# Optimization experiments

Measured on AMD Instinct MI355X. Metric: run time of the kernel, lower is better.

## Reference

```python
import jax, jax.numpy as jnp
import numpy as np

B = 8
N1, N2 = 65536, 16384
C1, C2 = 256, 512
BN_EPS = 1e-5


def setup_inputs() -> dict:
    key = jax.random.key(0)
    ks = jax.random.split(key, 8)
    xyz1 = jax.random.normal(ks[0], (N1, 3), dtype=jnp.float32)
    points1 = jax.random.normal(ks[1], (N1, C1), dtype=jnp.float32)
    xyz2 = jax.random.normal(ks[2], (N2, 3), dtype=jnp.float32)
    points2 = jax.random.normal(ks[3], (N2, C2), dtype=jnp.float32)
    offset1 = (jnp.arange(1, B + 1, dtype=jnp.int32) * (N1 // B))
    offset2 = (jnp.arange(1, B + 1, dtype=jnp.int32) * (N2 // B))
    W1 = jax.random.normal(ks[4], (C1 + C2, 256), dtype=jnp.float32) * 0.02
    b1 = jnp.zeros((256,), jnp.float32)
    g1 = jnp.ones((256,), jnp.float32)
    be1 = jnp.zeros((256,), jnp.float32)
    W2 = jax.random.normal(ks[5], (256, 256), dtype=jnp.float32) * 0.02
    b2 = jnp.zeros((256,), jnp.float32)
    g2 = jnp.ones((256,), jnp.float32)
    be2 = jnp.zeros((256,), jnp.float32)
    return dict(xyz1=xyz1, points1=points1, xyz2=xyz2, points2=points2,
                offset1=offset1, offset2=offset2,
                W1=W1, b1=b1, g1=g1, be1=be1, W2=W2, b2=b2, g2=g2, be2=be2)


def _knn3(q, k):
    # q: [n1,3] queries, k: [n2,3] reference set -> 3-NN idx + euclidean dist
    d2 = (jnp.sum(q * q, -1)[:, None] + jnp.sum(k * k, -1)[None, :]
          - 2.0 * (q @ k.T))                      # [n1, n2]
    neg_d2, idx = jax.lax.top_k(-d2, 3)           # [n1, 3]
    dist = jnp.sqrt(jnp.maximum(-neg_d2, 0.0))
    return idx, dist


def _bn_relu(x, g, be):
    # BatchNorm1d in training mode: biased batch stats over the point dim
    mu = jnp.mean(x, axis=0)
    var = jnp.mean((x - mu) ** 2, axis=0)
    return jax.nn.relu(g * (x - mu) * jax.lax.rsqrt(var + BN_EPS) + be)


def reference(xyz1, points1, xyz2, points2, offset1, offset2,
              W1, b1, g1, be1, W2, b2, g2, be2):
    bsz = offset1.shape[0]
    n1 = xyz1.shape[0] // bsz
    n2 = xyz2.shape[0] // bsz
    q = xyz1.reshape(bsz, n1, 3)
    k = xyz2.reshape(bsz, n2, 3)
    idx, dist = jax.vmap(_knn3)(q, k)             # [B,n1,3], [B,n1,3]
    gidx = (idx + (jnp.arange(bsz, dtype=idx.dtype) * n2)[:, None, None])
    gidx = gidx.reshape(-1, 3)                    # [N1,3] global row ids
    dist = dist.reshape(-1, 3)
    dist_recip = 1.0 / (dist + 1e-8)
    weight = dist_recip / jnp.sum(dist_recip, axis=1, keepdims=True)
    # fused gather + weighted accumulate: [N1,3,C2] * [N1,3,1] -> [N1,C2]
    interpolated = jnp.sum(points2[gidx] * weight[..., None], axis=1)
    x = jnp.concatenate([points1, interpolated], axis=1)  # [N1, C1+C2]
    x = _bn_relu(x @ W1 + b1, g1, be1)
    x = _bn_relu(x @ W2 + b2, g2, be2)
    return x
```

## Files before the change

kernel.cpp:

```cpp
#include <hip/hip_runtime.h>
#include <math.h>

#define N1T 65536
#define N2T 16384
#define BSZ 8
#define N1B 8192
#define N2B 2048
#define C1 256
#define C2 512
#define K1 768
#define HID 256
#define BN_EPS 1e-5f

typedef short bf16x8 __attribute__((ext_vector_type(8)));
typedef float f32x4 __attribute__((ext_vector_type(4)));

__device__ __forceinline__ float mul_rn(float a, float b) {
    float r; asm("v_mul_f32 %0, %1, %2" : "=v"(r) : "v"(a), "v"(b)); return r;
}
__device__ __forceinline__ float add_rn(float a, float b) {
    float r; asm("v_add_f32 %0, %1, %2" : "=v"(r) : "v"(a), "v"(b)); return r;
}
__device__ __forceinline__ float sub_rn(float a, float b) {
    float r; asm("v_sub_f32 %0, %1, %2" : "=v"(r) : "v"(a), "v"(b)); return r;
}
__device__ __forceinline__ float fma_rn(float a, float b, float c) {
    float r; asm("v_fma_f32 %0, %1, %2, %3" : "=v"(r) : "v"(a), "v"(b), "v"(c)); return r;
}
__device__ __forceinline__ short f2bf(float f) {
    unsigned u = __builtin_bit_cast(unsigned, f);
    u += 0x7fffu + ((u >> 16) & 1u);
    return (short)(u >> 16);
}
__device__ __forceinline__ float bf2f(short s) {
    return __builtin_bit_cast(float, ((unsigned)(unsigned short)s) << 16);
}

__global__ __launch_bounds__(256) void knn_kernel(
    const float* __restrict__ xyz1, const float* __restrict__ xyz2,
    int* __restrict__ idx_out, float* __restrict__ w_out)
{
    __shared__ float4 sref[N2B + 4];
    const int tid = threadIdx.x;
    const int qbase = blockIdx.x * 64;
    const int batch = qbase / N1B;
    const float* k2 = xyz2 + (size_t)batch * N2B * 3;
    for (int p = tid; p < N2B; p += 256) {
        float x = k2[3 * p], y = k2[3 * p + 1], z = k2[3 * p + 2];
        float kk = add_rn(add_rn(mul_rn(x, x), mul_rn(y, y)), mul_rn(z, z));
        sref[p + (p >> 9)] = make_float4(x, y, z, kk);
    }
    __syncthreads();

    const int q = qbase + (tid >> 2);
    const int sub = tid & 3;
    const float qx = xyz1[q * 3 + 0], qy = xyz1[q * 3 + 1], qz = xyz1[q * 3 + 2];
    const float qq = add_rn(add_rn(mul_rn(qx, qx), mul_rn(qy, qy)), mul_rn(qz, qz));

    const int base = sub * 513;
    const int gbase = sub * 512;
    float a0 = 1e30f, a1 = 1e30f, a2 = 1e30f;
    int   ai0 = 0x7fffffff, ai1 = 0x7fffffff, ai2 = 0x7fffffff;
    float c0 = 1e30f, c1 = 1e30f, c2 = 1e30f;
    int   ci0 = 0x7fffffff, ci1 = 0x7fffffff, ci2 = 0x7fffffff;
    for (int jj = 0; jj < 256; ++jj) {
        float4 rA = sref[base + jj];
        float4 rB = sref[base + 256 + jj];
        float pA = mul_rn(qx, rA.x);
        float tA = fma_rn(qz, rA.z, fma_rn(qy, rA.y, pA));
        float dA = add_rn(sub_rn(qq, add_rn(tA, tA)), rA.w);
        float pB = mul_rn(qx, rB.x);
        float tB = fma_rn(qz, rB.z, fma_rn(qy, rB.y, pB));
        float dB = add_rn(sub_rn(qq, add_rn(tB, tB)), rB.w);
        if (dA < a2) {
            if (dA < a1) {
                a2 = a1; ai2 = ai1;
                if (dA < a0) { a1 = a0; ai1 = ai0; a0 = dA; ai0 = gbase + jj; }
                else         { a1 = dA; ai1 = gbase + jj; }
            } else { a2 = dA; ai2 = gbase + jj; }
        }
        if (dB < c2) {
            if (dB < c1) {
                c2 = c1; ci2 = ci1;
                if (dB < c0) { c1 = c0; ci1 = ci0; c0 = dB; ci0 = gbase + 256 + jj; }
                else         { c1 = dB; ci1 = gbase + 256 + jj; }
            } else { c2 = dB; ci2 = gbase + 256 + jj; }
        }
    }
    float bd0 = a0, bd1 = a1, bd2 = a2;
    int   bi0 = ai0, bi1 = ai1, bi2 = ai2;
#define LEXINS(d, ji)                                                        \
    if ((d < bd2) || (d == bd2 && ji < bi2)) {                               \
        if ((d < bd1) || (d == bd1 && ji < bi1)) {                           \
            bd2 = bd1; bi2 = bi1;                                            \
            if ((d < bd0) || (d == bd0 && ji < bi0)) {                       \
                bd1 = bd0; bi1 = bi0; bd0 = d; bi0 = ji;                     \
            } else { bd1 = d; bi1 = ji; }                                    \
        } else { bd2 = d; bi2 = ji; }                                        \
    }
    LEXINS(c0, ci0) LEXINS(c1, ci1) LEXINS(c2, ci2)
#pragma unroll
    for (int mask = 1; mask <= 2; mask <<= 1) {
        float pd0 = __shfl_xor(bd0, mask, 64);
        float pd1 = __shfl_xor(bd1, mask, 64);
        float pd2 = __shfl_xor(bd2, mask, 64);
        int   pi0 = __shfl_xor(bi0, mask, 64);
        int   pi1 = __shfl_xor(bi1, mask, 64);
        int   pi2 = __shfl_xor(bi2, mask, 64);
        LEXINS(pd0, pi0) LEXINS(pd1, pi1) LEXINS(pd2, pi2)
    }
#undef LEXINS
    if (sub == 0) {
        float d0s = __fsqrt_rn(fmaxf(bd0, 0.0f));
        float d1s = __fsqrt_rn(fmaxf(bd1, 0.0f));
        float d2s = __fsqrt_rn(fmaxf(bd2, 0.0f));
        float r0 = __fdiv_rn(1.0f, add_rn(d0s, 1e-8f));
        float r1 = __fdiv_rn(1.0f, add_rn(d1s, 1e-8f));
        float r2 = __fdiv_rn(1.0f, add_rn(d2s, 1e-8f));
        float rs = add_rn(add_rn(r0, r1), r2);
        w_out[q * 3 + 0] = __fdiv_rn(r0, rs);
        w_out[q * 3 + 1] = __fdiv_rn(r1, rs);
        w_out[q * 3 + 2] = __fdiv_rn(r2, rs);
        idx_out[q * 3 + 0] = batch * N2B + bi0;
        idx_out[q * 3 + 1] = batch * N2B + bi1;
        idx_out[q * 3 + 2] = batch * N2B + bi2;
    }
}

__global__ __launch_bounds__(256) void cast_p2_kernel(
    const float* __restrict__ p2, short* __restrict__ p2b)
{
    const size_t i = ((size_t)blockIdx.x * 256 + threadIdx.x) * 8;
    float4 u0 = *(const float4*)(p2 + i);
    float4 u1 = *(const float4*)(p2 + i + 4);
    bf16x8 v;
    v[0] = f2bf(u0.x); v[1] = f2bf(u0.y); v[2] = f2bf(u0.z); v[3] = f2bf(u0.w);
    v[4] = f2bf(u1.x); v[5] = f2bf(u1.y); v[6] = f2bf(u1.z); v[7] = f2bf(u1.w);
    *(bf16x8*)(p2b + i) = v;
}

__global__ __launch_bounds__(256) void transpose_w_kernel(
    const float* __restrict__ Win, short* __restrict__ WT, int K, int N)
{
    const int e = blockIdx.x * 256 + threadIdx.x;
    const int k = e / N, n = e % N;
    WT[(size_t)n * K + k] = f2bf(Win[e]);
}

#define LDP 40

#define GEMM_EPILOGUE(STORE_STMT)                                             \
    __shared__ float redS[2][2][64], redQ[2][2][64];                          \
    _Pragma("unroll")                                                         \
    for (int n = 0; n < 4; ++n) {                                             \
        const int col = col0 + wc * 64 + n * 16 + l16;                        \
        const float bv = bias[col];                                           \
        float s = 0.f, qa = 0.f;                                              \
        _Pragma("unroll")                                                     \
        for (int m = 0; m < 4; ++m) {                                         \
            const int rowb = row0 + wr * 64 + m * 16 + (lane >> 4) * 4;       \
            _Pragma("unroll")                                                 \
            for (int j = 0; j < 4; ++j) {                                     \
                float v = acc[m][n][j] + bv;                                  \
                STORE_STMT;                                                   \
                s += v; qa = fmaf(v, v, qa);                                  \
            }                                                                 \
        }                                                                     \
        s += __shfl_xor(s, 16, 64);  s += __shfl_xor(s, 32, 64);              \
        qa += __shfl_xor(qa, 16, 64); qa += __shfl_xor(qa, 32, 64);           \
        if ((lane >> 4) == 0) {                                               \
            redS[wr][wc][n * 16 + l16] = s;                                   \
            redQ[wr][wc][n * 16 + l16] = qa;                                  \
        }                                                                     \
    }                                                                         \
    __syncthreads();                                                          \
    if (tid < 128) {                                                          \
        const int wcf = tid >> 6, cf = tid & 63;                              \
        float s = redS[0][wcf][cf] + redS[1][wcf][cf];                        \
        float qa = redQ[0][wcf][cf] + redQ[1][wcf][cf];                       \
        const int gcol = col0 + wcf * 64 + cf;                                \
        psum[(size_t)blockIdx.y * HID + gcol] = s;                            \
        psq[(size_t)blockIdx.y * HID + gcol] = qa;                            \
    }

__global__ __launch_bounds__(256) void gemm1m_kernel(
    const float* __restrict__ points1, const short* __restrict__ p2b,
    const int* __restrict__ idx, const float* __restrict__ w,
    const short* __restrict__ w1t, const float* __restrict__ bias,
    short* __restrict__ y1b, float* __restrict__ psum, float* __restrict__ psq)
{
    __shared__ short As[128][LDP];
    __shared__ short Bs[128][LDP];
    const int tid = threadIdx.x;
    const int lane = tid & 63, wv = tid >> 6;
    const int wr = wv >> 1, wc = wv & 1;
    const int l16 = lane & 15, kh = (lane >> 4) * 8;
    const int row0 = blockIdx.y * 128, col0 = blockIdx.x * 128;
    f32x4 acc[4][4];
#pragma unroll
    for (int m = 0; m < 4; ++m)
#pragma unroll
        for (int n = 0; n < 4; ++n) acc[m][n] = (f32x4){0.f, 0.f, 0.f, 0.f};

    const int c0 = tid * 2;
    const int r0c = c0 >> 2, kc0 = (c0 & 3) * 8;
    const int r1c = (c0 + 1) >> 2, kc1 = ((c0 + 1) & 3) * 8;

    const int   rowA = row0 + r0c,        rowB = row0 + r1c;
    const int   jA0 = idx[rowA * 3 + 0], jA1 = idx[rowA * 3 + 1], jA2 = idx[rowA * 3 + 2];
    const float wA0 = w[rowA * 3 + 0],   wA1 = w[rowA * 3 + 1],   wA2 = w[rowA * 3 + 2];
    const int   jB0 = idx[rowB * 3 + 0], jB1 = idx[rowB * 3 + 1], jB2 = idx[rowB * 3 + 2];
    const float wB0 = w[rowB * 3 + 0],   wB1 = w[rowB * 3 + 1],   wB2 = w[rowB * 3 + 2];

    for (int kt = 0; kt < K1 / 32; ++kt) {
        const int k0 = kt * 32;
        bf16x8 va, vb;
        if (k0 < C1) {
            float4 u0 = *(const float4*)(points1 + (size_t)rowA * C1 + k0 + kc0);
            float4 u1 = *(const float4*)(points1 + (size_t)rowA * C1 + k0 + kc0 + 4);
            va[0] = f2bf(u0.x); va[1] = f2bf(u0.y); va[2] = f2bf(u0.z); va[3] = f2bf(u0.w);
            va[4] = f2bf(u1.x); va[5] = f2bf(u1.y); va[6] = f2bf(u1.z); va[7] = f2bf(u1.w);
            float4 u2 = *(const float4*)(points1 + (size_t)rowB * C1 + k0 + kc1);
            float4 u3 = *(const float4*)(points1 + (size_t)rowB * C1 + k0 + kc1 + 4);
            vb[0] = f2bf(u2.x); vb[1] = f2bf(u2.y); vb[2] = f2bf(u2.z); vb[3] = f2bf(u2.w);
            vb[4] = f2bf(u3.x); vb[5] = f2bf(u3.y); vb[6] = f2bf(u3.z); vb[7] = f2bf(u3.w);
        } else {
            const int kbA = k0 - C1 + kc0, kbB = k0 - C1 + kc1;
            bf16x8 ga = *(const bf16x8*)(p2b + (size_t)jA0 * C2 + kbA);
            bf16x8 gb = *(const bf16x8*)(p2b + (size_t)jA1 * C2 + kbA);
            bf16x8 gc = *(const bf16x8*)(p2b + (size_t)jA2 * C2 + kbA);
#pragma unroll
            for (int e = 0; e < 8; ++e)
                va[e] = f2bf(fmaf(bf2f(ga[e]), wA0,
                         fmaf(bf2f(gb[e]), wA1, bf2f(gc[e]) * wA2)));
            bf16x8 gd = *(const bf16x8*)(p2b + (size_t)jB0 * C2 + kbB);
            bf16x8 ge = *(const bf16x8*)(p2b + (size_t)jB1 * C2 + kbB);
            bf16x8 gf = *(const bf16x8*)(p2b + (size_t)jB2 * C2 + kbB);
#pragma unroll
            for (int e = 0; e < 8; ++e)
                vb[e] = f2bf(fmaf(bf2f(gd[e]), wB0,
                         fmaf(bf2f(ge[e]), wB1, bf2f(gf[e]) * wB2)));
        }
        bf16x8 wa = *(const bf16x8*)(w1t + (size_t)(col0 + r0c) * K1 + k0 + kc0);
        bf16x8 wb = *(const bf16x8*)(w1t + (size_t)(col0 + r1c) * K1 + k0 + kc1);
        __syncthreads();
        *(bf16x8*)(&As[r0c][kc0]) = va;
        *(bf16x8*)(&As[r1c][kc1]) = vb;
        *(bf16x8*)(&Bs[r0c][kc0]) = wa;
        *(bf16x8*)(&Bs[r1c][kc1]) = wb;
        __syncthreads();

        bf16x8 af[4], bf[4];
#pragma unroll
        for (int m = 0; m < 4; ++m)
            af[m] = *(const bf16x8*)(&As[wr * 64 + m * 16 + l16][kh]);
#pragma unroll
        for (int n = 0; n < 4; ++n)
            bf[n] = *(const bf16x8*)(&Bs[wc * 64 + n * 16 + l16][kh]);
#pragma unroll
        for (int m = 0; m < 4; ++m)
#pragma unroll
            for (int n = 0; n < 4; ++n)
                acc[m][n] = __builtin_amdgcn_mfma_f32_16x16x32_bf16(
                    af[m], bf[n], acc[m][n], 0, 0, 0);
    }
    GEMM_EPILOGUE(y1b[(size_t)(rowb + j) * HID + col] = f2bf(v))
}

__global__ __launch_bounds__(256) void gemm2m_kernel(
    const short* __restrict__ y1b, const float* __restrict__ scale,
    const float* __restrict__ shift, const short* __restrict__ w2t,
    const float* __restrict__ bias, short* __restrict__ y2b,
    float* __restrict__ psum, float* __restrict__ psq)
{
    __shared__ short As[128][LDP];
    __shared__ short Bs[128][LDP];
    const int tid = threadIdx.x;
    const int lane = tid & 63, wv = tid >> 6;
    const int wr = wv >> 1, wc = wv & 1;
    const int l16 = lane & 15, kh = (lane >> 4) * 8;
    const int row0 = blockIdx.y * 128, col0 = blockIdx.x * 128;
    f32x4 acc[4][4];
#pragma unroll
    for (int m = 0; m < 4; ++m)
#pragma unroll
        for (int n = 0; n < 4; ++n) acc[m][n] = (f32x4){0.f, 0.f, 0.f, 0.f};

    const int c0 = tid * 2;
    const int r0c = c0 >> 2, kc0 = (c0 & 3) * 8;
    const int r1c = (c0 + 1) >> 2, kc1 = ((c0 + 1) & 3) * 8;

    for (int kt = 0; kt < HID / 32; ++kt) {
        const int k0 = kt * 32;
        bf16x8 x0 = *(const bf16x8*)(y1b + (size_t)(row0 + r0c) * HID + k0 + kc0);
        bf16x8 x1 = *(const bf16x8*)(y1b + (size_t)(row0 + r1c) * HID + k0 + kc1);
        float4 s0 = *(const float4*)(scale + k0 + kc0);
        float4 s1 = *(const float4*)(scale + k0 + kc0 + 4);
        float4 h0 = *(const float4*)(shift + k0 + kc0);
        float4 h1 = *(const float4*)(shift + k0 + kc0 + 4);
        float4 s2 = *(const float4*)(scale + k0 + kc1);
        float4 s3 = *(const float4*)(scale + k0 + kc1 + 4);
        float4 h2 = *(const float4*)(shift + k0 + kc1);
        float4 h3 = *(const float4*)(shift + k0 + kc1 + 4);
        bf16x8 va, vb;
        va[0] = f2bf(fmaxf(fmaf(bf2f(x0[0]), s0.x, h0.x), 0.f));
        va[1] = f2bf(fmaxf(fmaf(bf2f(x0[1]), s0.y, h0.y), 0.f));
        va[2] = f2bf(fmaxf(fmaf(bf2f(x0[2]), s0.z, h0.z), 0.f));
        va[3] = f2bf(fmaxf(fmaf(bf2f(x0[3]), s0.w, h0.w), 0.f));
        va[4] = f2bf(fmaxf(fmaf(bf2f(x0[4]), s1.x, h1.x), 0.f));
        va[5] = f2bf(fmaxf(fmaf(bf2f(x0[5]), s1.y, h1.y), 0.f));
        va[6] = f2bf(fmaxf(fmaf(bf2f(x0[6]), s1.z, h1.z), 0.f));
        va[7] = f2bf(fmaxf(fmaf(bf2f(x0[7]), s1.w, h1.w), 0.f));
        vb[0] = f2bf(fmaxf(fmaf(bf2f(x1[0]), s2.x, h2.x), 0.f));
        vb[1] = f2bf(fmaxf(fmaf(bf2f(x1[1]), s2.y, h2.y), 0.f));
        vb[2] = f2bf(fmaxf(fmaf(bf2f(x1[2]), s2.z, h2.z), 0.f));
        vb[3] = f2bf(fmaxf(fmaf(bf2f(x1[3]), s2.w, h2.w), 0.f));
        vb[4] = f2bf(fmaxf(fmaf(bf2f(x1[4]), s3.x, h3.x), 0.f));
        vb[5] = f2bf(fmaxf(fmaf(bf2f(x1[5]), s3.y, h3.y), 0.f));
        vb[6] = f2bf(fmaxf(fmaf(bf2f(x1[6]), s3.z, h3.z), 0.f));
        vb[7] = f2bf(fmaxf(fmaf(bf2f(x1[7]), s3.w, h3.w), 0.f));
        bf16x8 wa = *(const bf16x8*)(w2t + (size_t)(col0 + r0c) * HID + k0 + kc0);
        bf16x8 wb = *(const bf16x8*)(w2t + (size_t)(col0 + r1c) * HID + k0 + kc1);
        __syncthreads();
        *(bf16x8*)(&As[r0c][kc0]) = va;
        *(bf16x8*)(&As[r1c][kc1]) = vb;
        *(bf16x8*)(&Bs[r0c][kc0]) = wa;
        *(bf16x8*)(&Bs[r1c][kc1]) = wb;
        __syncthreads();

        bf16x8 af[4], bf[4];
#pragma unroll
        for (int m = 0; m < 4; ++m)
            af[m] = *(const bf16x8*)(&As[wr * 64 + m * 16 + l16][kh]);
#pragma unroll
        for (int n = 0; n < 4; ++n)
            bf[n] = *(const bf16x8*)(&Bs[wc * 64 + n * 16 + l16][kh]);
#pragma unroll
        for (int m = 0; m < 4; ++m)
#pragma unroll
            for (int n = 0; n < 4; ++n)
                acc[m][n] = __builtin_amdgcn_mfma_f32_16x16x32_bf16(
                    af[m], bf[n], acc[m][n], 0, 0, 0);
    }
    GEMM_EPILOGUE(y2b[(size_t)(rowb + j) * HID + col] = f2bf(v))
}

__global__ __launch_bounds__(256) void bn_finalize_kernel(
    const float* __restrict__ psum, const float* __restrict__ psq,
    const float* __restrict__ g, const float* __restrict__ be,
    float* __restrict__ scale, float* __restrict__ shift)
{
    const int c = threadIdx.x;
    float s = 0.0f, q = 0.0f;
    for (int b = 0; b < 512; ++b) { s += psum[b * HID + c]; q += psq[b * HID + c]; }
    const float inv_n = 1.0f / (float)N1T;
    const float mu = s * inv_n;
    const float var = fmaxf(q * inv_n - mu * mu, 0.0f);
    const float sc = g[c] * rsqrtf(var + BN_EPS);
    scale[c] = sc;
    shift[c] = be[c] - mu * sc;
}

__global__ __launch_bounds__(256) void bn_apply_kernel(
    const short* __restrict__ y2b, const float* __restrict__ scale,
    const float* __restrict__ shift, float* __restrict__ out)
{
    const size_t i = ((size_t)blockIdx.x * 256 + threadIdx.x) * 8;
    const int c8 = (int)(i & 255);
    bf16x8 x = *(const bf16x8*)(y2b + i);
    float4 s0 = *(const float4*)(scale + c8);
    float4 s1 = *(const float4*)(scale + c8 + 4);
    float4 h0 = *(const float4*)(shift + c8);
    float4 h1 = *(const float4*)(shift + c8 + 4);
    float4 o0, o1;
    o0.x = fmaxf(fmaf(bf2f(x[0]), s0.x, h0.x), 0.f);
    o0.y = fmaxf(fmaf(bf2f(x[1]), s0.y, h0.y), 0.f);
    o0.z = fmaxf(fmaf(bf2f(x[2]), s0.z, h0.z), 0.f);
    o0.w = fmaxf(fmaf(bf2f(x[3]), s0.w, h0.w), 0.f);
    o1.x = fmaxf(fmaf(bf2f(x[4]), s1.x, h1.x), 0.f);
    o1.y = fmaxf(fmaf(bf2f(x[5]), s1.y, h1.y), 0.f);
    o1.z = fmaxf(fmaf(bf2f(x[6]), s1.z, h1.z), 0.f);
    o1.w = fmaxf(fmaf(bf2f(x[7]), s1.w, h1.w), 0.f);
    *(float4*)(out + i) = o0;
    *(float4*)(out + i + 4) = o1;
}

extern "C" void kernel_launch(void* const* d_in, const int* in_sizes, int n_in,
                              void* d_out, int out_size, void* d_ws, size_t ws_size,
                              hipStream_t stream)
{
    const float* xyz1    = (const float*)d_in[0];
    const float* points1 = (const float*)d_in[1];
    const float* xyz2    = (const float*)d_in[2];
    const float* points2 = (const float*)d_in[3];
    const float* W1  = (const float*)d_in[6];
    const float* b1  = (const float*)d_in[7];
    const float* g1  = (const float*)d_in[8];
    const float* be1 = (const float*)d_in[9];
    const float* W2  = (const float*)d_in[10];
    const float* b2  = (const float*)d_in[11];
    const float* g2  = (const float*)d_in[12];
    const float* be2 = (const float*)d_in[13];
    float* out = (float*)d_out;

    char* ws = (char*)d_ws;
    short* y1b  = (short*)ws;
    short* y2b  = (short*)(ws + 33554432);
    short* p2b  = (short*)(ws + 67108864);
    size_t off  = 67108864 + 16777216;
    short*  w1t    = (short*)(ws + off);  off += (size_t)K1 * HID * 2;
    short*  w2t    = (short*)(ws + off);  off += (size_t)HID * HID * 2;
    int*    idx    = (int*)(ws + off);    off += (size_t)N1T * 3 * 4;
    float*  w      = (float*)(ws + off);  off += (size_t)N1T * 3 * 4;
    float*  psum   = (float*)(ws + off);  off += 512 * 256 * 4;
    float*  psq    = (float*)(ws + off);  off += 512 * 256 * 4;
    float*  scale1 = (float*)(ws + off);  off += 256 * 4;
    float*  shift1 = (float*)(ws + off);  off += 256 * 4;
    float*  scale2 = (float*)(ws + off);  off += 256 * 4;
    float*  shift2 = (float*)(ws + off);  off += 256 * 4;

    cast_p2_kernel<<<N2T * C2 / 8 / 256, 256, 0, stream>>>(points2, p2b);
    transpose_w_kernel<<<K1 * HID / 256, 256, 0, stream>>>(W1, w1t, K1, HID);
    transpose_w_kernel<<<HID * HID / 256, 256, 0, stream>>>(W2, w2t, HID, HID);
    knn_kernel<<<1024, 256, 0, stream>>>(xyz1, xyz2, idx, w);
    gemm1m_kernel<<<dim3(HID / 128, N1T / 128), 256, 0, stream>>>(
        points1, p2b, idx, w, w1t, b1, y1b, psum, psq);
    bn_finalize_kernel<<<1, 256, 0, stream>>>(psum, psq, g1, be1, scale1, shift1);
    gemm2m_kernel<<<dim3(HID / 128, N1T / 128), 256, 0, stream>>>(
        y1b, scale1, shift1, w2t, b2, y2b, psum, psq);
    bn_finalize_kernel<<<1, 256, 0, stream>>>(psum, psq, g2, be2, scale2, shift2);
    bn_apply_kernel<<<N1T * HID / 8 / 256, 256, 0, stream>>>(y2b, scale2, shift2, out);
}
```

Measured before the change: 274.5 us.

## Widen gemm1 tile to full 256 columns and prefetch next K-tile into registers

The first fused gather+GEMM kernel now uses 512-thread blocks that each compute a 128x256 output tile, covering all hidden columns. The points1 load and the 3-neighbour gather/interpolation for a row block therefore happen once instead of twice, one per column block. The loop also loads the next K-tile's A and B values into registers while the current tile's MFMAs run, giving software prefetch across the barrier. The cost is more LDS per block, half as many blocks, and higher register pressure from the prefetched values.

```diff
diff --git a/kernel.cpp b/kernel.cpp
--- a/kernel.cpp
+++ b/kernel.cpp
@@ -148,6 +148,121 @@
 }
 
 #define LDP 40
+
+__global__ __launch_bounds__(512) void gemm1m_kernel(
+    const float* __restrict__ points1, const short* __restrict__ p2b,
+    const int* __restrict__ idx, const float* __restrict__ w,
+    const short* __restrict__ w1t, const float* __restrict__ bias,
+    short* __restrict__ y1b, float* __restrict__ psum, float* __restrict__ psq)
+{
+    __shared__ short As[128][LDP];
+    __shared__ short Bs[256][LDP];
+    __shared__ float redS[2][4][64], redQ[2][4][64];
+    const int tid = threadIdx.x;
+    const int lane = tid & 63, wv = tid >> 6;
+    const int wr = wv >> 2, wc = wv & 3;
+    const int l16 = lane & 15, kh = (lane >> 4) * 8;
+    const int row0 = blockIdx.x * 128;
+    f32x4 acc[4][4];
+#pragma unroll
+    for (int m = 0; m < 4; ++m)
+#pragma unroll
+        for (int n = 0; n < 4; ++n) acc[m][n] = (f32x4){0.f, 0.f, 0.f, 0.f};
+
+    const int arow = tid >> 2, akc = (tid & 3) * 8;
+    const int rowA = row0 + arow;
+    const int   jA0 = idx[rowA * 3 + 0], jA1 = idx[rowA * 3 + 1], jA2 = idx[rowA * 3 + 2];
+    const float wA0 = w[rowA * 3 + 0],   wA1 = w[rowA * 3 + 1],   wA2 = w[rowA * 3 + 2];
+    const int cb0 = tid * 2, cb1 = tid * 2 + 1;
+    const int brow0 = cb0 >> 2, bkc0 = (cb0 & 3) * 8;
+    const int brow1 = cb1 >> 2, bkc1 = (cb1 & 3) * 8;
+
+#define LOAD_A(VA, KT)                                                        \
+    {                                                                         \
+        const int k0_ = (KT) * 32;                                            \
+        if (k0_ < C1) {                                                       \
+            float4 u0 = *(const float4*)(points1 + (size_t)rowA * C1 + k0_ + akc);     \
+            float4 u1 = *(const float4*)(points1 + (size_t)rowA * C1 + k0_ + akc + 4); \
+            VA[0] = f2bf(u0.x); VA[1] = f2bf(u0.y); VA[2] = f2bf(u0.z); VA[3] = f2bf(u0.w); \
+            VA[4] = f2bf(u1.x); VA[5] = f2bf(u1.y); VA[6] = f2bf(u1.z); VA[7] = f2bf(u1.w); \
+        } else {                                                              \
+            const int kb = k0_ - C1 + akc;                                    \
+            bf16x8 ga = *(const bf16x8*)(p2b + (size_t)jA0 * C2 + kb);        \
+            bf16x8 gb = *(const bf16x8*)(p2b + (size_t)jA1 * C2 + kb);        \
+            bf16x8 gc = *(const bf16x8*)(p2b + (size_t)jA2 * C2 + kb);        \
+            _Pragma("unroll")                                                 \
+            for (int e = 0; e < 8; ++e)                                       \
+                VA[e] = f2bf(fmaf(bf2f(ga[e]), wA0,                           \
+                          fmaf(bf2f(gb[e]), wA1, bf2f(gc[e]) * wA2)));        \
+        }                                                                     \
+    }
+#define LOAD_B(WA, WB, KT)                                                    \
+    {                                                                         \
+        const int k0_ = (KT) * 32;                                            \
+        WA = *(const bf16x8*)(w1t + (size_t)brow0 * K1 + k0_ + bkc0);         \
+        WB = *(const bf16x8*)(w1t + (size_t)brow1 * K1 + k0_ + bkc1);         \
+    }
+
+    bf16x8 va, wa, wb;
+    LOAD_A(va, 0)
+    LOAD_B(wa, wb, 0)
+    for (int kt = 0; kt < K1 / 32; ++kt) {
+        __syncthreads();
+        *(bf16x8*)(&As[arow][akc]) = va;
+        *(bf16x8*)(&Bs[brow0][bkc0]) = wa;
+        *(bf16x8*)(&Bs[brow1][bkc1]) = wb;
+        __syncthreads();
+        if (kt + 1 < K1 / 32) {
+            LOAD_A(va, kt + 1)
+            LOAD_B(wa, wb, kt + 1)
+        }
+        bf16x8 af[4], bf[4];
+#pragma unroll
+        for (int m = 0; m < 4; ++m)
+            af[m] = *(const bf16x8*)(&As[wr * 64 + m * 16 + l16][kh]);
+#pragma unroll
+        for (int n = 0; n < 4; ++n)
+            bf[n] = *(const bf16x8*)(&Bs[wc * 64 + n * 16 + l16][kh]);
+#pragma unroll
+        for (int m = 0; m < 4; ++m)
+#pragma unroll
+            for (int n = 0; n < 4; ++n)
+                acc[m][n] = __builtin_amdgcn_mfma_f32_16x16x32_bf16(
+                    af[m], bf[n], acc[m][n], 0, 0, 0);
+    }
+#undef LOAD_A
+#undef LOAD_B
+#pragma unroll
+    for (int n = 0; n < 4; ++n) {
+        const int col = wc * 64 + n * 16 + l16;
+        const float bv = bias[col];
+        float s = 0.f, qa = 0.f;
+#pragma unroll
+        for (int m = 0; m < 4; ++m) {
+            const int rowb = row0 + wr * 64 + m * 16 + (lane >> 4) * 4;
+#pragma unroll
+            for (int j = 0; j < 4; ++j) {
+                float v = acc[m][n][j] + bv;
+                y1b[(size_t)(rowb + j) * HID + col] = f2bf(v);
+                s += v; qa = fmaf(v, v, qa);
+            }
+        }
+        s += __shfl_xor(s, 16, 64);  s += __shfl_xor(s, 32, 64);
+        qa += __shfl_xor(qa, 16, 64); qa += __shfl_xor(qa, 32, 64);
+        if ((lane >> 4) == 0) {
+            redS[wr][wc][n * 16 + l16] = s;
+            redQ[wr][wc][n * 16 + l16] = qa;
+        }
+    }
+    __syncthreads();
+    if (tid < 256) {
+        const int wcf = tid >> 6, cf = tid & 63;
+        float s = redS[0][wcf][cf] + redS[1][wcf][cf];
+        float qa = redQ[0][wcf][cf] + redQ[1][wcf][cf];
+        psum[(size_t)blockIdx.x * HID + tid] = s;
+        psq[(size_t)blockIdx.x * HID + tid] = qa;
+    }
+}
 
 #define GEMM_EPILOGUE(STORE_STMT)                                             \
     __shared__ float redS[2][2][64], redQ[2][2][64];                          \
@@ -182,90 +297,6 @@
         psum[(size_t)blockIdx.y * HID + gcol] = s;                            \
         psq[(size_t)blockIdx.y * HID + gcol] = qa;                            \
     }
-
-__global__ __launch_bounds__(256) void gemm1m_kernel(
-    const float* __restrict__ points1, const short* __restrict__ p2b,
-    const int* __restrict__ idx, const float* __restrict__ w,
-    const short* __restrict__ w1t, const float* __restrict__ bias,
-    short* __restrict__ y1b, float* __restrict__ psum, float* __restrict__ psq)
-{
-    __shared__ short As[128][LDP];
-    __shared__ short Bs[128][LDP];
-    const int tid = threadIdx.x;
-    const int lane = tid & 63, wv = tid >> 6;
-    const int wr = wv >> 1, wc = wv & 1;
-    const int l16 = lane & 15, kh = (lane >> 4) * 8;
-    const int row0 = blockIdx.y * 128, col0 = blockIdx.x * 128;
-    f32x4 acc[4][4];
-#pragma unroll
-    for (int m = 0; m < 4; ++m)
-#pragma unroll
-        for (int n = 0; n < 4; ++n) acc[m][n] = (f32x4){0.f, 0.f, 0.f, 0.f};
-
-    const int c0 = tid * 2;
-    const int r0c = c0 >> 2, kc0 = (c0 & 3) * 8;
-    const int r1c = (c0 + 1) >> 2, kc1 = ((c0 + 1) & 3) * 8;
-
-    const int   rowA = row0 + r0c,        rowB = row0 + r1c;
-    const int   jA0 = idx[rowA * 3 + 0], jA1 = idx[rowA * 3 + 1], jA2 = idx[rowA * 3 + 2];
-    const float wA0 = w[rowA * 3 + 0],   wA1 = w[rowA * 3 + 1],   wA2 = w[rowA * 3 + 2];
-    const int   jB0 = idx[rowB * 3 + 0], jB1 = idx[rowB * 3 + 1], jB2 = idx[rowB * 3 + 2];
-    const float wB0 = w[rowB * 3 + 0],   wB1 = w[rowB * 3 + 1],   wB2 = w[rowB * 3 + 2];
-
-    for (int kt = 0; kt < K1 / 32; ++kt) {
-        const int k0 = kt * 32;
-        bf16x8 va, vb;
-        if (k0 < C1) {
-            float4 u0 = *(const float4*)(points1 + (size_t)rowA * C1 + k0 + kc0);
-            float4 u1 = *(const float4*)(points1 + (size_t)rowA * C1 + k0 + kc0 + 4);
-            va[0] = f2bf(u0.x); va[1] = f2bf(u0.y); va[2] = f2bf(u0.z); va[3] = f2bf(u0.w);
-            va[4] = f2bf(u1.x); va[5] = f2bf(u1.y); va[6] = f2bf(u1.z); va[7] = f2bf(u1.w);
-            float4 u2 = *(const float4*)(points1 + (size_t)rowB * C1 + k0 + kc1);
-            float4 u3 = *(const float4*)(points1 + (size_t)rowB * C1 + k0 + kc1 + 4);
-            vb[0] = f2bf(u2.x); vb[1] = f2bf(u2.y); vb[2] = f2bf(u2.z); vb[3] = f2bf(u2.w);
-            vb[4] = f2bf(u3.x); vb[5] = f2bf(u3.y); vb[6] = f2bf(u3.z); vb[7] = f2bf(u3.w);
-        } else {
-            const int kbA = k0 - C1 + kc0, kbB = k0 - C1 + kc1;
-            bf16x8 ga = *(const bf16x8*)(p2b + (size_t)jA0 * C2 + kbA);
-            bf16x8 gb = *(const bf16x8*)(p2b + (size_t)jA1 * C2 + kbA);
-            bf16x8 gc = *(const bf16x8*)(p2b + (size_t)jA2 * C2 + kbA);
-#pragma unroll
-            for (int e = 0; e < 8; ++e)
-                va[e] = f2bf(fmaf(bf2f(ga[e]), wA0,
-                         fmaf(bf2f(gb[e]), wA1, bf2f(gc[e]) * wA2)));
-            bf16x8 gd = *(const bf16x8*)(p2b + (size_t)jB0 * C2 + kbB);
-            bf16x8 ge = *(const bf16x8*)(p2b + (size_t)jB1 * C2 + kbB);
-            bf16x8 gf = *(const bf16x8*)(p2b + (size_t)jB2 * C2 + kbB);
-#pragma unroll
-            for (int e = 0; e < 8; ++e)
-                vb[e] = f2bf(fmaf(bf2f(gd[e]), wB0,
-                         fmaf(bf2f(ge[e]), wB1, bf2f(gf[e]) * wB2)));
-        }
-        bf16x8 wa = *(const bf16x8*)(w1t + (size_t)(col0 + r0c) * K1 + k0 + kc0);
-        bf16x8 wb = *(const bf16x8*)(w1t + (size_t)(col0 + r1c) * K1 + k0 + kc1);
-        __syncthreads();
-        *(bf16x8*)(&As[r0c][kc0]) = va;
-        *(bf16x8*)(&As[r1c][kc1]) = vb;
-        *(bf16x8*)(&Bs[r0c][kc0]) = wa;
-        *(bf16x8*)(&Bs[r1c][kc1]) = wb;
-        __syncthreads();
-
-        bf16x8 af[4], bf[4];
-#pragma unroll
-        for (int m = 0; m < 4; ++m)
-            af[m] = *(const bf16x8*)(&As[wr * 64 + m * 16 + l16][kh]);
-#pragma unroll
-        for (int n = 0; n < 4; ++n)
-            bf[n] = *(const bf16x8*)(&Bs[wc * 64 + n * 16 + l16][kh]);
-#pragma unroll
-        for (int m = 0; m < 4; ++m)
-#pragma unroll
-            for (int n = 0; n < 4; ++n)
-                acc[m][n] = __builtin_amdgcn_mfma_f32_16x16x32_bf16(
-                    af[m], bf[n], acc[m][n], 0, 0, 0);
-    }
-    GEMM_EPILOGUE(y1b[(size_t)(rowb + j) * HID + col] = f2bf(v))
-}
 
 __global__ __launch_bounds__(256) void gemm2m_kernel(
     const short* __restrict__ y1b, const float* __restrict__ scale,
@@ -423,7 +454,7 @@
     transpose_w_kernel<<<K1 * HID / 256, 256, 0, stream>>>(W1, w1t, K1, HID);
     transpose_w_kernel<<<HID * HID / 256, 256, 0, stream>>>(W2, w2t, HID, HID);
     knn_kernel<<<1024, 256, 0, stream>>>(xyz1, xyz2, idx, w);
-    gemm1m_kernel<<<dim3(HID / 128, N1T / 128), 256, 0, stream>>>(
+    gemm1m_kernel<<<N1T / 128, 512, 0, stream>>>(
         points1, p2b, idx, w, w1t, b1, y1b, psum, psq);
     bn_finalize_kernel<<<1, 256, 0, stream>>>(psum, psq, g1, be1, scale1, shift1);
     gemm2m_kernel<<<dim3(HID / 128, N1T / 128), 256, 0, stream>>>(
```

Result: faster. 233.3 us (-15.0%).
